# Kernel optimization log

Measured on AMD Instinct MI355X. Metric: run time of the kernel, lower is better.

The kernel has to match this reference:

```python
import jax, jax.numpy as jnp
import numpy as np

B, S, E, H = 4, 2048, 1024, 16
D = E // H  # head dim = 64

def setup_inputs() -> dict:
    key = jax.random.key(0)
    k1, k2, k3 = jax.random.split(key, 3)
    scale = 0.02
    return {
        "x": jax.random.normal(k1, (B, S, E), dtype=jnp.float32),
        "W_qkv": jax.random.normal(k2, (E, 3 * E), dtype=jnp.float32) * scale,
        "b_qkv": jnp.zeros((3 * E,), dtype=jnp.float32),
        "W_o": jax.random.normal(k3, (E, E), dtype=jnp.float32) * scale,
        "b_o": jnp.zeros((E,), dtype=jnp.float32),
    }

def reference(x, W_qkv, b_qkv, W_o, b_o):
    # dropout is identity in eval mode
    qkv = x @ W_qkv + b_qkv                      # [B, S, 3E]
    q, k, v = jnp.split(qkv, 3, axis=-1)          # each [B, S, E]
    def split_heads(t):
        return t.reshape(B, S, H, D).transpose(0, 2, 1, 3)  # [B, H, S, D]
    q, k, v = split_heads(q), split_heads(k), split_heads(v)
    scores = jnp.einsum("bhsd,bhtd->bhst", q, k) / jnp.sqrt(jnp.float32(D))
    causal = jnp.tril(jnp.ones((S, S), dtype=bool))
    scores = jnp.where(causal[None, None], scores, jnp.float32(-jnp.inf))
    attn = jax.nn.softmax(scores, axis=-1)        # [B, H, S, S]
    out = jnp.einsum("bhst,bhtd->bhsd", attn, v)  # [B, H, S, D]
    out = out.transpose(0, 2, 1, 3).reshape(B, S, E)
    return out @ W_o + b_o
```

## Files before the change

### kernel.cpp

```cpp
#include <hip/hip_runtime.h>
#include <stdint.h>

typedef __bf16 bf16_t;
typedef __bf16 bf16x8 __attribute__((ext_vector_type(8)));
typedef float f32x4 __attribute__((ext_vector_type(4)));

#define LOG2E 1.44269504088896340736f

__device__ __forceinline__ float fexp2(float x) {
#if __has_builtin(__builtin_amdgcn_exp2f)
    return __builtin_amdgcn_exp2f(x);
#else
    return exp2f(x);
#endif
}

__device__ __forceinline__ void gld_lds16(const bf16_t* g, bf16_t* l) {
    __builtin_amdgcn_global_load_lds(
        (__attribute__((address_space(1))) void*)(bf16_t*)g,
        (__attribute__((address_space(3))) void*)l,
        16, 0, 0);
}

__global__ __launch_bounds__(256) void prep_k(
    const float* __restrict__ x, bf16_t* __restrict__ xb,
    const float* __restrict__ Wqkv, bf16_t* __restrict__ wqkvT,
    const float* __restrict__ Wo, bf16_t* __restrict__ woT)
{
    __shared__ float t[32][33];
    const int tid = threadIdx.x;
    int blk = blockIdx.x;
    if (blk < 8192) {
        int i = blk * 1024 + tid * 4;
        float4 v = *(const float4*)(x + i);
        union { bf16_t b[4]; uint2 u; } u;
        u.b[0] = (bf16_t)v.x; u.b[1] = (bf16_t)v.y; u.b[2] = (bf16_t)v.z; u.b[3] = (bf16_t)v.w;
        *(uint2*)(xb + i) = u.u;
        return;
    }
    const float* in; bf16_t* out; int C, bx, by;
    if (blk < 11264) { blk -= 8192; in = Wqkv; out = wqkvT; C = 3072; bx = blk % 96; by = blk / 96; }
    else             { blk -= 11264; in = Wo;   out = woT;   C = 1024; bx = blk % 32; by = blk / 32; }
    const int R = 1024;
    const int tx = tid & 31, ty = tid >> 5;
    const int c0 = bx * 32, r0 = by * 32;
    #pragma unroll
    for (int j = 0; j < 32; j += 8)
        t[ty + j][tx] = in[(size_t)(r0 + ty + j) * C + c0 + tx];
    __syncthreads();
    #pragma unroll
    for (int j = 0; j < 32; j += 8)
        out[(size_t)(c0 + ty + j) * R + r0 + tx] = (bf16_t)t[tx][ty + j];
}

__device__ __forceinline__ void gemm128_body(
    const bf16_t* __restrict__ A, const bf16_t* __restrict__ Bt,
    bf16_t* Al, bf16_t* Bl, f32x4 (&acc)[4][4], int m0, int n0, int Kd)
{
    const int tid = threadIdx.x;
    const int w = tid >> 6, lane = tid & 63;
    const int l15 = lane & 15, quad = lane >> 4;
    const int wm = w >> 1, wn = w & 1;

    const int srow = lane >> 3;
    const int scg = ((lane & 7) ^ srow) * 8;
    const bf16_t* Ag = A + (size_t)(m0 + w * 32 + srow) * Kd + scg;
    const bf16_t* Bg = Bt + (size_t)(n0 + w * 32 + srow) * Kd + scg;
    bf16_t* Ald = Al + (w * 32) * 64;
    bf16_t* Bld = Bl + (w * 32) * 64;

    const int rc0 = (quad ^ (l15 & 7)) * 8;
    const int rc1 = ((quad + 4) ^ (l15 & 7)) * 8;

    for (int k0 = 0; k0 < Kd; k0 += 64) {
        __syncthreads();
        #pragma unroll
        for (int j = 0; j < 4; j++) {
            gld_lds16(Ag + k0 + (size_t)(j * 8) * Kd, Ald + (j * 8) * 64);
            gld_lds16(Bg + k0 + (size_t)(j * 8) * Kd, Bld + (j * 8) * 64);
        }
        __syncthreads();

        #pragma unroll
        for (int hh = 0; hh < 2; hh++) {
            const int rc = hh ? rc1 : rc0;
            bf16x8 af[4], bf[4];
            #pragma unroll
            for (int mi = 0; mi < 4; mi++)
                af[mi] = *(const bf16x8*)(Al + (wm * 64 + mi * 16 + l15) * 64 + rc);
            #pragma unroll
            for (int ni = 0; ni < 4; ni++)
                bf[ni] = *(const bf16x8*)(Bl + (wn * 64 + ni * 16 + l15) * 64 + rc);
            #pragma unroll
            for (int mi = 0; mi < 4; mi++)
                #pragma unroll
                for (int ni = 0; ni < 4; ni++)
                    acc[mi][ni] = __builtin_amdgcn_mfma_f32_16x16x32_bf16(
                        af[mi], bf[ni], acc[mi][ni], 0, 0, 0);
        }
    }
}

__global__ __launch_bounds__(256) void gemm_qkv_k(
    const bf16_t* __restrict__ X, const bf16_t* __restrict__ WT,
    const float* __restrict__ bias,
    bf16_t* __restrict__ Qb, bf16_t* __restrict__ Kb, bf16_t* __restrict__ VTb)
{
    __shared__ bf16_t Al[128 * 64];
    __shared__ bf16_t Bl[128 * 64];
    const int tid = threadIdx.x;
    const int lane = tid & 63, w = tid >> 6;
    const int l15 = lane & 15, quad = lane >> 4;
    const int wm = w >> 1, wn = w & 1;
    const int n0 = blockIdx.x * 128;
    const int m0 = blockIdx.y * 128;

    f32x4 acc[4][4];
    #pragma unroll
    for (int mi = 0; mi < 4; mi++)
        #pragma unroll
        for (int ni = 0; ni < 4; ni++) acc[mi][ni] = (f32x4){0.f, 0.f, 0.f, 0.f};

    gemm128_body(WT, X, Al, Bl, acc, m0, n0, 1024);

    const float QSCALE = 0.125f * LOG2E;
    const int region = m0 >> 10;
    #pragma unroll
    for (int mi = 0; mi < 4; mi++) {
        const int mbase = m0 + wm * 64 + mi * 16 + quad * 4;
        const float4 bia = *(const float4*)(bias + mbase);
        const float ba[4] = {bia.x, bia.y, bia.z, bia.w};
        const int col = mbase & 1023;
        const int h = col >> 6, dbase = col & 63;
        #pragma unroll
        for (int ni = 0; ni < 4; ni++) {
            const int n = n0 + wn * 64 + ni * 16 + l15;
            const int b = n >> 11, s = n & 2047;
            if (region == 0) {
                union { bf16_t bv[4]; uint2 u; } u;
                #pragma unroll
                for (int r = 0; r < 4; r++)
                    u.bv[r] = (bf16_t)((acc[mi][ni][r] + ba[r]) * QSCALE);
                *(uint2*)(Qb + (((size_t)b * 16 + h) * 2048 + s) * 64 + dbase) = u.u;
            } else if (region == 1) {
                union { bf16_t bv[4]; uint2 u; } u;
                #pragma unroll
                for (int r = 0; r < 4; r++)
                    u.bv[r] = (bf16_t)(acc[mi][ni][r] + ba[r]);
                *(uint2*)(Kb + (((size_t)b * 16 + h) * 2048 + s) * 64 + dbase) = u.u;
            } else {
                bf16_t* dst = VTb + (((size_t)b * 16 + h) * 64 + dbase) * 2048 + s;
                #pragma unroll
                for (int r = 0; r < 4; r++)
                    dst[(size_t)r * 2048] = (bf16_t)(acc[mi][ni][r] + ba[r]);
            }
        }
    }
}

__global__ __launch_bounds__(256) void attn_k(
    const bf16_t* __restrict__ Qb, const bf16_t* __restrict__ Kb,
    const bf16_t* __restrict__ VTb, bf16_t* __restrict__ Ob)
{
    __shared__ bf16_t Kl[64 * 64];
    __shared__ bf16_t Vl[64 * 64];
    __shared__ bf16_t Pl[4][16 * 72];

    const int tid = threadIdx.x;
    const int w = tid >> 6, lane = tid & 63;
    const int l15 = lane & 15, quad = lane >> 4;
    const int idx = blockIdx.x;
    const int qt = 31 - (idx >> 6);
    const int bh = idx & 63;
    const int b = bh >> 4, h = bh & 15;
    const int q0 = qt * 64;

    const bf16_t* Qp = Qb + (size_t)bh * 2048 * 64;
    const bf16_t* Kp = Kb + (size_t)bh * 2048 * 64;
    const bf16_t* Vp = VTb + (size_t)bh * 64 * 2048;

    const int srow = w * 16 + (lane >> 3);
    const int scol = ((lane & 7) ^ ((lane >> 3) & 7)) * 8;
    const int rc0 = (quad ^ (l15 & 7)) * 8;
    const int rc1 = ((quad + 4) ^ (l15 & 7)) * 8;

    const int qrow = q0 + w * 16 + l15;
    bf16x8 aq0 = *(const bf16x8*)(Qp + (size_t)qrow * 64 + quad * 8);
    bf16x8 aq1 = *(const bf16x8*)(Qp + (size_t)qrow * 64 + 32 + quad * 8);

    bf16x8 vone;
    #pragma unroll
    for (int j = 0; j < 8; j++) vone[j] = (bf16_t)1.0f;

    f32x4 o[4];
    #pragma unroll
    for (int ni = 0; ni < 4; ni++) o[ni] = (f32x4){0.f, 0.f, 0.f, 0.f};
    f32x4 lacc = (f32x4){0.f, 0.f, 0.f, 0.f};
    const int qloc = w * 16 + l15;

    for (int kv0 = 0; kv0 <= q0; kv0 += 64) {
        __syncthreads();
        gld_lds16(Kp + (size_t)(kv0 + srow) * 64 + scol, Kl + (w * 16) * 64);
        gld_lds16(Kp + (size_t)(kv0 + srow + 8) * 64 + scol, Kl + (w * 16 + 8) * 64);
        gld_lds16(Vp + (size_t)srow * 2048 + kv0 + scol, Vl + (w * 16) * 64);
        gld_lds16(Vp + (size_t)(srow + 8) * 2048 + kv0 + scol, Vl + (w * 16 + 8) * 64);
        __syncthreads();

        f32x4 sv[4];
        #pragma unroll
        for (int ni = 0; ni < 4; ni++) {
            bf16x8 ak0 = *(const bf16x8*)(Kl + (ni * 16 + l15) * 64 + rc0);
            bf16x8 ak1 = *(const bf16x8*)(Kl + (ni * 16 + l15) * 64 + rc1);
            f32x4 z = (f32x4){0.f, 0.f, 0.f, 0.f};
            z = __builtin_amdgcn_mfma_f32_16x16x32_bf16(ak0, aq0, z, 0, 0, 0);
            z = __builtin_amdgcn_mfma_f32_16x16x32_bf16(ak1, aq1, z, 0, 0, 0);
            sv[ni] = z;
        }

        if (kv0 == q0) {
            #pragma unroll
            for (int ni = 0; ni < 4; ni++)
                #pragma unroll
                for (int r = 0; r < 4; r++)
                    if (ni * 16 + quad * 4 + r > qloc) sv[ni][r] = -INFINITY;
        }

        #pragma unroll
        for (int ni = 0; ni < 4; ni++) {
            union { bf16_t bv[4]; uint2 u; } pk;
            #pragma unroll
            for (int r = 0; r < 4; r++) pk.bv[r] = (bf16_t)fexp2(sv[ni][r]);
            *(uint2*)(&Pl[w][l15 * 72 + ni * 16 + quad * 4]) = pk.u;
        }

        bf16x8 pa0 = *(const bf16x8*)(&Pl[w][l15 * 72 + quad * 8]);
        bf16x8 pa1 = *(const bf16x8*)(&Pl[w][l15 * 72 + 32 + quad * 8]);
        #pragma unroll
        for (int ni = 0; ni < 4; ni++) {
            bf16x8 bv0 = *(const bf16x8*)(Vl + (ni * 16 + l15) * 64 + rc0);
            bf16x8 bv1 = *(const bf16x8*)(Vl + (ni * 16 + l15) * 64 + rc1);
            o[ni] = __builtin_amdgcn_mfma_f32_16x16x32_bf16(bv0, pa0, o[ni], 0, 0, 0);
            o[ni] = __builtin_amdgcn_mfma_f32_16x16x32_bf16(bv1, pa1, o[ni], 0, 0, 0);
        }
        lacc = __builtin_amdgcn_mfma_f32_16x16x32_bf16(vone, pa0, lacc, 0, 0, 0);
        lacc = __builtin_amdgcn_mfma_f32_16x16x32_bf16(vone, pa1, lacc, 0, 0, 0);
    }

    const float inv = 1.0f / lacc[0];
    const int s = q0 + w * 16 + l15;
    bf16_t* obase = Ob + ((size_t)b * 2048 + s) * 1024 + h * 64;
    #pragma unroll
    for (int ni = 0; ni < 4; ni++) {
        union { bf16_t bv[4]; uint2 u; } u;
        #pragma unroll
        for (int r = 0; r < 4; r++) u.bv[r] = (bf16_t)(o[ni][r] * inv);
        *(uint2*)(obase + ni * 16 + quad * 4) = u.u;
    }
}

__global__ __launch_bounds__(256) void gemm_out_k(
    const bf16_t* __restrict__ O, const bf16_t* __restrict__ WT,
    const float* __restrict__ bias, float* __restrict__ out)
{
    __shared__ bf16_t Al[128 * 64];
    __shared__ bf16_t Bl[128 * 64];
    const int tid = threadIdx.x;
    const int lane = tid & 63, w = tid >> 6;
    const int l15 = lane & 15, quad = lane >> 4;
    const int wm = w >> 1, wn = w & 1;
    const int n0 = blockIdx.x * 128;
    const int m0 = blockIdx.y * 128;

    f32x4 acc[4][4];
    #pragma unroll
    for (int mi = 0; mi < 4; mi++)
        #pragma unroll
        for (int ni = 0; ni < 4; ni++) acc[mi][ni] = (f32x4){0.f, 0.f, 0.f, 0.f};

    gemm128_body(WT, O, Al, Bl, acc, m0, n0, 1024);

    #pragma unroll
    for (int mi = 0; mi < 4; mi++) {
        const int mbase = m0 + wm * 64 + mi * 16 + quad * 4;
        const float4 bia = *(const float4*)(bias + mbase);
        #pragma unroll
        for (int ni = 0; ni < 4; ni++) {
            const int n = n0 + wn * 64 + ni * 16 + l15;
            float4 v;
            v.x = acc[mi][ni][0] + bia.x;
            v.y = acc[mi][ni][1] + bia.y;
            v.z = acc[mi][ni][2] + bia.z;
            v.w = acc[mi][ni][3] + bia.w;
            *(float4*)(out + (size_t)n * 1024 + mbase) = v;
        }
    }
}


extern "C" void kernel_launch(void* const* d_in, const int* in_sizes, int n_in,
                              void* d_out, int out_size, void* d_ws, size_t ws_size,
                              hipStream_t stream) {
    const float* x     = (const float*)d_in[0];
    const float* W_qkv = (const float*)d_in[1];
    const float* b_qkv = (const float*)d_in[2];
    const float* W_o   = (const float*)d_in[3];
    const float* b_o   = (const float*)d_in[4];
    float* out = (float*)d_out;

    char* ws = (char*)d_ws;
    size_t off = 0;
    auto alloc = [&](size_t bytes) -> void* {
        void* p = ws + off;
        off += (bytes + 255) & ~(size_t)255;
        return p;
    };
    bf16_t* xb    = (bf16_t*)alloc((size_t)8192 * 1024 * 2);
    bf16_t* wqkvT = (bf16_t*)alloc((size_t)3072 * 1024 * 2);
    bf16_t* woT   = (bf16_t*)alloc((size_t)1024 * 1024 * 2);
    bf16_t* Qb    = (bf16_t*)alloc((size_t)8192 * 1024 * 2);
    bf16_t* Kb    = (bf16_t*)alloc((size_t)8192 * 1024 * 2);
    bf16_t* VTb   = (bf16_t*)alloc((size_t)8192 * 1024 * 2);
    bf16_t* Ob    = xb;

    prep_k<<<12288, 256, 0, stream>>>(x, xb, W_qkv, wqkvT, W_o, woT);
    gemm_qkv_k<<<dim3(64, 24), 256, 0, stream>>>(xb, wqkvT, b_qkv, Qb, Kb, VTb);
    attn_k<<<2048, 256, 0, stream>>>(Qb, Kb, VTb, Ob);
    gemm_out_k<<<dim3(64, 8), 256, 0, stream>>>(Ob, woT, b_o, out);
}
```

Before: 236.9 us.

## Process two query tiles per attention block and shrink output GEMM M-tile

The attention kernel now gives each block 128 query rows, two 64-row sub-tiles per wave, so every K/V tile loaded into LDS feeds twice as many MFMAs. This halves the number of blocks and cuts redundant K/V traffic. The cost is more registers and a doubled P buffer, plus one extra wasted KV iteration of masked work on the diagonal. Separately, the output GEMM drops from 128x128 to 64x128 tiles with its own inline loop, doubling the grid to improve occupancy and wave count on a small GEMM.

```diff
diff --git a/kernel.cpp b/kernel.cpp
--- a/kernel.cpp
+++ b/kernel.cpp
@@ -164,16 +164,16 @@
 {
     __shared__ bf16_t Kl[64 * 64];
     __shared__ bf16_t Vl[64 * 64];
-    __shared__ bf16_t Pl[4][16 * 72];
+    __shared__ bf16_t Pl[4][2 * 16 * 72];
 
     const int tid = threadIdx.x;
     const int w = tid >> 6, lane = tid & 63;
     const int l15 = lane & 15, quad = lane >> 4;
     const int idx = blockIdx.x;
-    const int qt = 31 - (idx >> 6);
+    const int qt = 15 - (idx >> 6);
     const int bh = idx & 63;
     const int b = bh >> 4, h = bh & 15;
-    const int q0 = qt * 64;
+    const int q0 = qt * 128;
 
     const bf16_t* Qp = Qb + (size_t)bh * 2048 * 64;
     const bf16_t* Kp = Kb + (size_t)bh * 2048 * 64;
@@ -184,21 +184,27 @@
     const int rc0 = (quad ^ (l15 & 7)) * 8;
     const int rc1 = ((quad + 4) ^ (l15 & 7)) * 8;
 
-    const int qrow = q0 + w * 16 + l15;
-    bf16x8 aq0 = *(const bf16x8*)(Qp + (size_t)qrow * 64 + quad * 8);
-    bf16x8 aq1 = *(const bf16x8*)(Qp + (size_t)qrow * 64 + 32 + quad * 8);
+    bf16x8 aq[2][2];
+    #pragma unroll
+    for (int qa = 0; qa < 2; qa++) {
+        const size_t qrow = q0 + qa * 64 + w * 16 + l15;
+        aq[qa][0] = *(const bf16x8*)(Qp + qrow * 64 + quad * 8);
+        aq[qa][1] = *(const bf16x8*)(Qp + qrow * 64 + 32 + quad * 8);
+    }
 
     bf16x8 vone;
     #pragma unroll
     for (int j = 0; j < 8; j++) vone[j] = (bf16_t)1.0f;
 
-    f32x4 o[4];
-    #pragma unroll
-    for (int ni = 0; ni < 4; ni++) o[ni] = (f32x4){0.f, 0.f, 0.f, 0.f};
-    f32x4 lacc = (f32x4){0.f, 0.f, 0.f, 0.f};
+    f32x4 o[2][4];
+    #pragma unroll
+    for (int qa = 0; qa < 2; qa++)
+        #pragma unroll
+        for (int ni = 0; ni < 4; ni++) o[qa][ni] = (f32x4){0.f, 0.f, 0.f, 0.f};
+    f32x4 lacc[2] = {(f32x4){0.f, 0.f, 0.f, 0.f}, (f32x4){0.f, 0.f, 0.f, 0.f}};
     const int qloc = w * 16 + l15;
 
-    for (int kv0 = 0; kv0 <= q0; kv0 += 64) {
+    for (int kv0 = 0; kv0 <= q0 + 64; kv0 += 64) {
         __syncthreads();
         gld_lds16(Kp + (size_t)(kv0 + srow) * 64 + scol, Kl + (w * 16) * 64);
         gld_lds16(Kp + (size_t)(kv0 + srow + 8) * 64 + scol, Kl + (w * 16 + 8) * 64);
@@ -206,55 +212,81 @@
         gld_lds16(Vp + (size_t)(srow + 8) * 2048 + kv0 + scol, Vl + (w * 16 + 8) * 64);
         __syncthreads();
 
-        f32x4 sv[4];
+        f32x4 sv[2][4];
         #pragma unroll
         for (int ni = 0; ni < 4; ni++) {
             bf16x8 ak0 = *(const bf16x8*)(Kl + (ni * 16 + l15) * 64 + rc0);
             bf16x8 ak1 = *(const bf16x8*)(Kl + (ni * 16 + l15) * 64 + rc1);
-            f32x4 z = (f32x4){0.f, 0.f, 0.f, 0.f};
-            z = __builtin_amdgcn_mfma_f32_16x16x32_bf16(ak0, aq0, z, 0, 0, 0);
-            z = __builtin_amdgcn_mfma_f32_16x16x32_bf16(ak1, aq1, z, 0, 0, 0);
-            sv[ni] = z;
-        }
-
-        if (kv0 == q0) {
+            #pragma unroll
+            for (int qa = 0; qa < 2; qa++) {
+                f32x4 z = (f32x4){0.f, 0.f, 0.f, 0.f};
+                z = __builtin_amdgcn_mfma_f32_16x16x32_bf16(ak0, aq[qa][0], z, 0, 0, 0);
+                z = __builtin_amdgcn_mfma_f32_16x16x32_bf16(ak1, aq[qa][1], z, 0, 0, 0);
+                sv[qa][ni] = z;
+            }
+        }
+
+        if (kv0 >= q0) {
+            const int qaD = (kv0 > q0) ? 1 : 0;
             #pragma unroll
             for (int ni = 0; ni < 4; ni++)
                 #pragma unroll
                 for (int r = 0; r < 4; r++)
-                    if (ni * 16 + quad * 4 + r > qloc) sv[ni][r] = -INFINITY;
-        }
-
-        #pragma unroll
-        for (int ni = 0; ni < 4; ni++) {
-            union { bf16_t bv[4]; uint2 u; } pk;
-            #pragma unroll
-            for (int r = 0; r < 4; r++) pk.bv[r] = (bf16_t)fexp2(sv[ni][r]);
-            *(uint2*)(&Pl[w][l15 * 72 + ni * 16 + quad * 4]) = pk.u;
-        }
-
-        bf16x8 pa0 = *(const bf16x8*)(&Pl[w][l15 * 72 + quad * 8]);
-        bf16x8 pa1 = *(const bf16x8*)(&Pl[w][l15 * 72 + 32 + quad * 8]);
+                    if (ni * 16 + quad * 4 + r > qloc) sv[qaD][ni][r] = -INFINITY;
+            if (kv0 > q0) {
+                #pragma unroll
+                for (int ni = 0; ni < 4; ni++)
+                    #pragma unroll
+                    for (int r = 0; r < 4; r++) sv[0][ni][r] = -INFINITY;
+            }
+        }
+
+        #pragma unroll
+        for (int qa = 0; qa < 2; qa++)
+            #pragma unroll
+            for (int ni = 0; ni < 4; ni++) {
+                union { bf16_t bv[4]; uint2 u; } pk;
+                #pragma unroll
+                for (int r = 0; r < 4; r++) pk.bv[r] = (bf16_t)fexp2(sv[qa][ni][r]);
+                *(uint2*)(&Pl[w][(qa * 16 + l15) * 72 + ni * 16 + quad * 4]) = pk.u;
+            }
+
+        bf16x8 pa[2][2];
+        #pragma unroll
+        for (int qa = 0; qa < 2; qa++) {
+            pa[qa][0] = *(const bf16x8*)(&Pl[w][(qa * 16 + l15) * 72 + quad * 8]);
+            pa[qa][1] = *(const bf16x8*)(&Pl[w][(qa * 16 + l15) * 72 + 32 + quad * 8]);
+        }
+
         #pragma unroll
         for (int ni = 0; ni < 4; ni++) {
             bf16x8 bv0 = *(const bf16x8*)(Vl + (ni * 16 + l15) * 64 + rc0);
             bf16x8 bv1 = *(const bf16x8*)(Vl + (ni * 16 + l15) * 64 + rc1);
-            o[ni] = __builtin_amdgcn_mfma_f32_16x16x32_bf16(bv0, pa0, o[ni], 0, 0, 0);
-            o[ni] = __builtin_amdgcn_mfma_f32_16x16x32_bf16(bv1, pa1, o[ni], 0, 0, 0);
-        }
-        lacc = __builtin_amdgcn_mfma_f32_16x16x32_bf16(vone, pa0, lacc, 0, 0, 0);
-        lacc = __builtin_amdgcn_mfma_f32_16x16x32_bf16(vone, pa1, lacc, 0, 0, 0);
-    }
-
-    const float inv = 1.0f / lacc[0];
-    const int s = q0 + w * 16 + l15;
-    bf16_t* obase = Ob + ((size_t)b * 2048 + s) * 1024 + h * 64;
-    #pragma unroll
-    for (int ni = 0; ni < 4; ni++) {
-        union { bf16_t bv[4]; uint2 u; } u;
-        #pragma unroll
-        for (int r = 0; r < 4; r++) u.bv[r] = (bf16_t)(o[ni][r] * inv);
-        *(uint2*)(obase + ni * 16 + quad * 4) = u.u;
+            #pragma unroll
+            for (int qa = 0; qa < 2; qa++) {
+                o[qa][ni] = __builtin_amdgcn_mfma_f32_16x16x32_bf16(bv0, pa[qa][0], o[qa][ni], 0, 0, 0);
+                o[qa][ni] = __builtin_amdgcn_mfma_f32_16x16x32_bf16(bv1, pa[qa][1], o[qa][ni], 0, 0, 0);
+            }
+        }
+        #pragma unroll
+        for (int qa = 0; qa < 2; qa++) {
+            lacc[qa] = __builtin_amdgcn_mfma_f32_16x16x32_bf16(vone, pa[qa][0], lacc[qa], 0, 0, 0);
+            lacc[qa] = __builtin_amdgcn_mfma_f32_16x16x32_bf16(vone, pa[qa][1], lacc[qa], 0, 0, 0);
+        }
+    }
+
+    #pragma unroll
+    for (int qa = 0; qa < 2; qa++) {
+        const float inv = 1.0f / lacc[qa][0];
+        const int s = q0 + qa * 64 + w * 16 + l15;
+        bf16_t* obase = Ob + ((size_t)b * 2048 + s) * 1024 + h * 64;
+        #pragma unroll
+        for (int ni = 0; ni < 4; ni++) {
+            union { bf16_t bv[4]; uint2 u; } u;
+            #pragma unroll
+            for (int r = 0; r < 4; r++) u.bv[r] = (bf16_t)(o[qa][ni][r] * inv);
+            *(uint2*)(obase + ni * 16 + quad * 4) = u.u;
+        }
     }
 }
 
@@ -262,26 +294,62 @@
     const bf16_t* __restrict__ O, const bf16_t* __restrict__ WT,
     const float* __restrict__ bias, float* __restrict__ out)
 {
-    __shared__ bf16_t Al[128 * 64];
+    __shared__ bf16_t Al[64 * 64];
     __shared__ bf16_t Bl[128 * 64];
     const int tid = threadIdx.x;
     const int lane = tid & 63, w = tid >> 6;
     const int l15 = lane & 15, quad = lane >> 4;
     const int wm = w >> 1, wn = w & 1;
     const int n0 = blockIdx.x * 128;
-    const int m0 = blockIdx.y * 128;
-
-    f32x4 acc[4][4];
-    #pragma unroll
-    for (int mi = 0; mi < 4; mi++)
+    const int m0 = blockIdx.y * 64;
+
+    const int srow = lane >> 3;
+    const int scg = ((lane & 7) ^ srow) * 8;
+    const bf16_t* Ag = WT + (size_t)(m0 + w * 16 + srow) * 1024 + scg;
+    const bf16_t* Bg = O + (size_t)(n0 + w * 32 + srow) * 1024 + scg;
+    bf16_t* Ald = Al + (w * 16) * 64;
+    bf16_t* Bld = Bl + (w * 32) * 64;
+
+    const int rc0 = (quad ^ (l15 & 7)) * 8;
+    const int rc1 = ((quad + 4) ^ (l15 & 7)) * 8;
+
+    f32x4 acc[2][4];
+    #pragma unroll
+    for (int mi = 0; mi < 2; mi++)
         #pragma unroll
         for (int ni = 0; ni < 4; ni++) acc[mi][ni] = (f32x4){0.f, 0.f, 0.f, 0.f};
 
-    gemm128_body(WT, O, Al, Bl, acc, m0, n0, 1024);
-
-    #pragma unroll
-    for (int mi = 0; mi < 4; mi++) {
-        const int mbase = m0 + wm * 64 + mi * 16 + quad * 4;
+    for (int k0 = 0; k0 < 1024; k0 += 64) {
+        __syncthreads();
+        gld_lds16(Ag + k0, Ald);
+        gld_lds16(Ag + k0 + (size_t)8 * 1024, Ald + 8 * 64);
+        #pragma unroll
+        for (int j = 0; j < 4; j++)
+            gld_lds16(Bg + k0 + (size_t)(j * 8) * 1024, Bld + (j * 8) * 64);
+        __syncthreads();
+
+        #pragma unroll
+        for (int hh = 0; hh < 2; hh++) {
+            const int rc = hh ? rc1 : rc0;
+            bf16x8 af[2], bf[4];
+            #pragma unroll
+            for (int mi = 0; mi < 2; mi++)
+                af[mi] = *(const bf16x8*)(Al + (wm * 32 + mi * 16 + l15) * 64 + rc);
+            #pragma unroll
+            for (int ni = 0; ni < 4; ni++)
+                bf[ni] = *(const bf16x8*)(Bl + (wn * 64 + ni * 16 + l15) * 64 + rc);
+            #pragma unroll
+            for (int mi = 0; mi < 2; mi++)
+                #pragma unroll
+                for (int ni = 0; ni < 4; ni++)
+                    acc[mi][ni] = __builtin_amdgcn_mfma_f32_16x16x32_bf16(
+                        af[mi], bf[ni], acc[mi][ni], 0, 0, 0);
+        }
+    }
+
+    #pragma unroll
+    for (int mi = 0; mi < 2; mi++) {
+        const int mbase = m0 + wm * 32 + mi * 16 + quad * 4;
         const float4 bia = *(const float4*)(bias + mbase);
         #pragma unroll
         for (int ni = 0; ni < 4; ni++) {
@@ -324,6 +392,6 @@
 
     prep_k<<<12288, 256, 0, stream>>>(x, xb, W_qkv, wqkvT, W_o, woT);
     gemm_qkv_k<<<dim3(64, 24), 256, 0, stream>>>(xb, wqkvT, b_qkv, Qb, Kb, VTb);
-    attn_k<<<2048, 256, 0, stream>>>(Qb, Kb, VTb, Ob);
-    gemm_out_k<<<dim3(64, 8), 256, 0, stream>>>(Ob, woT, b_o, out);
-}
+    attn_k<<<1024, 256, 0, stream>>>(Qb, Kb, VTb, Ob);
+    gemm_out_k<<<dim3(64, 16), 256, 0, stream>>>(Ob, woT, b_o, out);
+}
```

Result: slower. 254.0 us (+7.2%).
